# Optimization experiments

Measured on AMD Instinct MI355X. Metric: run time of the kernel, lower is better.

## Reference

```python
import jax, jax.numpy as jnp
import numpy as np

BN_EPS = 1e-5

def _sqdist(a, b):
    # a: (B,N,3), b: (B,M,3) -> (B,N,M)
    return (jnp.sum(a**2, -1)[:, :, None] + jnp.sum(b**2, -1)[:, None, :]
            - 2.0 * jnp.einsum('bnc,bmc->bnm', a, b))

def _knn_idx(pts, k):
    # smallest-k neighbor indices, (B,N,k)
    d = _sqdist(pts, pts)
    _, idx = jax.lax.top_k(-d, k)
    return idx

def _group(feat, idx):
    # feat (B,C,N), idx (B,N,K) -> (B,C,N,K)
    return jax.vmap(lambda f, i: f[:, i])(feat, idx)

def _gather_pts(pts, idx):
    # pts (B,M,C), idx (B,...) -> (B,...,C)
    return jax.vmap(lambda p, i: p[i])(pts, idx)

def _conv1(w, b, x):
    # 1x1 conv1d: w (O,C), x (B,C,N)
    return jnp.einsum('oc,bcn->bon', w, x) + b[None, :, None]

def _conv2(w, x, b=None):
    # 1x1 conv2d: w (O,C), x (B,C,N,K)
    y = jnp.einsum('oc,bcnk->bonk', w, x)
    return y if b is None else y + b[None, :, None, None]

def _bn_eval(x, gamma, beta):
    # eval-mode BatchNorm2d with running_mean=0, running_var=1
    s = gamma / jnp.sqrt(1.0 + BN_EPS)
    return x * s[None, :, None, None] + beta[None, :, None, None]

def _lgrp(x_q, x, P_anchor, map_idx, anchor_dist, lw1, lw2, lw3, k=16):
    # x_q, x: (B,n,3) -> weights (B,dim,n,k)
    d = _sqdist(x_q, x)
    _, idx = jax.lax.top_k(-d, k)                      # (B,n,k)
    neighbors = _gather_pts(x, idx)                    # (B,n,k,3)
    R1 = jnp.abs(x_q[:, :, None, :] - neighbors)       # (B,n,k,3)
    B_idx = _gather_pts(map_idx[..., None], idx)[..., 0]  # (B,n,k)
    anchorA = _gather_pts(P_anchor, map_idx)           # (B,n,3)
    anchorB = _gather_pts(P_anchor, B_idx)             # (B,n,k,3)
    dA = jnp.linalg.norm(x_q - anchorA, axis=-1)       # (B,n)
    dB = jnp.linalg.norm(neighbors - anchorB, axis=-1) # (B,n,k)
    dAB = jax.vmap(lambda ad, a, bi: ad[a[:, None], bi])(anchor_dist, map_idx, B_idx)
    R2s = dA[:, :, None] + dAB + dB                    # (B,n,k)
    R2 = jnp.broadcast_to(R2s[..., None], R1.shape)
    feats = jnp.concatenate([R1, R2], axis=-1).transpose(0, 3, 1, 2)  # (B,6,n,k)
    h = jax.nn.relu(_conv2(lw1, feats))
    h = jax.nn.relu(_conv2(lw2, h))
    return _conv2(lw3, h)                              # (B,dim,n,k)

def setup_inputs() -> dict:
    key = jax.random.key(0)
    ks = jax.random.split(key, 32)
    B, C_in, n, dim, M, k = 2, 128, 2048, 256, 128, 16
    hid_p, hid_a = 64, dim * 4
    s = 0.05
    inp = {
        'x': jax.random.normal(ks[0], (B, C_in, n), jnp.float32),
        'pos': jax.random.normal(ks[1], (B, 3, n), jnp.float32),
        'fps_idx': jax.random.randint(ks[2], (B, n), 0, n),
        'P_anchor': jax.random.normal(ks[3], (B, M, 3), jnp.float32),
        'map_idx': jax.random.randint(ks[4], (B, n), 0, M),
        'anchor_dist': jax.random.uniform(ks[5], (B, M, M), jnp.float32) * 2.0,
        'w_start': jax.random.normal(ks[6], (dim, C_in)) * s,
        'b_start': jnp.zeros((dim,), jnp.float32),
        'w_key': jax.random.normal(ks[7], (dim, dim)) * s,
        'b_key': jnp.zeros((dim,), jnp.float32),
        'w_query': jax.random.normal(ks[8], (dim, dim)) * s,
        'b_query': jnp.zeros((dim,), jnp.float32),
        'w_value': jax.random.normal(ks[9], (dim, dim)) * s,
        'b_value': jnp.zeros((dim,), jnp.float32),
        'pw1': jax.random.normal(ks[10], (hid_p, 3)) * s,
        'pb1': jnp.zeros((hid_p,), jnp.float32),
        'pg1': jnp.ones((hid_p,), jnp.float32),
        'pbt1': jnp.zeros((hid_p,), jnp.float32),
        'pw2': jax.random.normal(ks[11], (dim, hid_p)) * s,
        'pb2': jnp.zeros((dim,), jnp.float32),
        'lw1': jax.random.normal(ks[12], (32, 6)) * s,
        'lw2': jax.random.normal(ks[13], (64, 32)) * s,
        'lw3': jax.random.normal(ks[14], (dim, 64)) * s,
        'aw1': jax.random.normal(ks[15], (hid_a, dim)) * s,
        'ab1': jnp.zeros((hid_a,), jnp.float32),
        'ag1': jnp.ones((hid_a,), jnp.float32),
        'abt1': jnp.zeros((hid_a,), jnp.float32),
        'aw2': jax.random.normal(ks[16], (dim, hid_a)) * s,
        'ab2': jnp.zeros((dim,), jnp.float32),
        'w_end': jax.random.normal(ks[17], (C_in, dim)) * s,
        'b_end': jnp.zeros((C_in,), jnp.float32),
    }
    return inp

def reference(x, pos, fps_idx, P_anchor, map_idx, anchor_dist,
              w_start, b_start, w_key, b_key, w_query, b_query, w_value, b_value,
              pw1, pb1, pg1, pbt1, pw2, pb2, lw1, lw2, lw3,
              aw1, ab1, ag1, abt1, aw2, ab2, w_end, b_end):
    n_knn = 16
    identity = x
    xf = _conv1(w_start, b_start, x)                   # (B,dim,n)
    pos_f = pos.transpose(0, 2, 1)                     # (B,n,3)
    idx_knn = _knn_idx(pos_f, n_knn)                   # (B,n,k)
    key_f = _conv1(w_key, b_key, xf)
    value = _conv1(w_value, b_value, xf)
    query = _conv1(w_query, b_query, xf)
    key_g = _group(key_f, idx_knn)                     # (B,dim,n,k)
    qk_rel = query[:, :, :, None] - key_g
    pos_rel = pos[:, :, :, None] - _group(pos, idx_knn)
    f_l = _lgrp(pos_f, pos_f, P_anchor, map_idx, anchor_dist, lw1, lw2, lw3, k=16)
    # pos_mlp: conv-bn-relu-conv
    h = _bn_eval(_conv2(pw1, pos_rel, pb1), pg1, pbt1)
    pos_emb = _conv2(pw2, jax.nn.relu(h), pb2)         # (B,dim,n,k)
    # attn_mlp
    a = _bn_eval(_conv2(aw1, qk_rel + pos_emb + f_l, ab1), ag1, abt1)
    attention = _conv2(aw2, jax.nn.relu(a), ab2)
    attention = jax.nn.softmax(attention, axis=-1)
    value_e = value[:, :, :, None] + pos_emb + f_l
    agg = jnp.sum(attention * value_e, axis=-1)        # (B,dim,n)
    y = _conv1(w_end, b_end, agg)
    return y + identity
```

## Files before the change

### kernel.cpp

```cpp
#include <hip/hip_runtime.h>
#include <hip/hip_bf16.h>

typedef __hip_bfloat16 bf16;
typedef unsigned short u16;
typedef __attribute__((ext_vector_type(8))) short s8v;
typedef __attribute__((ext_vector_type(4))) float f32x4;

#define NP    2048
#define DC    256
#define MA    128
#define KNN_  16
#define LKV   768

#define MFMA_B16(a,b,c) __builtin_amdgcn_mfma_f32_16x16x32_bf16(a,b,c,0,0,0)

__device__ __forceinline__ float u2f(u16 u){ return __uint_as_float(((unsigned int)u)<<16); }
__device__ __forceinline__ u16 f2u(float f){ bf16 h=__float2bfloat16(f); u16 us; __builtin_memcpy(&us,&h,2); return us; }

__device__ __forceinline__ s8v ldpk(const u16* pk, int rb, int KS, int ks, int l){
  return *(const s8v*)(pk + (((size_t)((rb*KS + ks)*64 + l))<<3));
}

__device__ __forceinline__ s8v ldF(const u16* base, int cf, int ks, int NKS, int l){
  return *(const s8v*)((const char*)base + (((cf*NKS + ks)<<10) | (l<<4)));
}
__device__ __forceinline__ int faddr(int col, int ch, int NKS){
  int cf = col>>4, ks = ch>>5, lane = (((ch>>3)&3)<<4)|(col&15), j = ch&7;
  return ((cf*NKS + ks)<<10) + (lane<<4) + (j<<1);
}
__device__ __forceinline__ void stF4(u16* base, int col, int ch0, int NKS,
                                     float v0, float v1, float v2, float v3){
  uint2 pkv;
  pkv.x = (unsigned)f2u(v0) | ((unsigned)f2u(v1)<<16);
  pkv.y = (unsigned)f2u(v2) | ((unsigned)f2u(v3)<<16);
  *(uint2*)((char*)base + faddr(col, ch0, NKS)) = pkv;
}
__device__ __forceinline__ void stF1(u16* base, int col, int ch, int NKS, float v){
  *(u16*)((char*)base + faddr(col, ch, NKS)) = f2u(v);
}
__device__ __forceinline__ void ldF4(const u16* base, int col, int ch0, int NKS, float* o){
  uint2 pkv = *(const uint2*)((const char*)base + faddr(col, ch0, NKS));
  o[0] = u2f(pkv.x & 0xffff); o[1] = u2f(pkv.x>>16);
  o[2] = u2f(pkv.y & 0xffff); o[3] = u2f(pkv.y>>16);
}

__global__ __launch_bounds__(256) void kqv_fused(
    const u16* __restrict__ wstpk, const float* __restrict__ b_start,
    const u16* __restrict__ wkqvpk, const float* __restrict__ bkqv,
    const float* __restrict__ x, float* __restrict__ kqvT)
{
  __shared__ u16 Bx[64*128];
  __shared__ u16 Bt[64*256];
  const int tid = threadIdx.x;
  const int w = tid>>6, l = tid&63, k = l&15, g = l>>4;
  const int n0 = blockIdx.x*64, m0 = blockIdx.y*128, bb = blockIdx.z;
  for (int e = tid*4; e < 64*128; e += 1024) {
    int kk = e >> 6, c = e & 63;
    float4 v = *(const float4*)(x + (size_t)bb*128*NP + (size_t)kk*NP + n0 + c);
    stF1(Bx, c+0, kk, 4, v.x); stF1(Bx, c+1, kk, 4, v.y);
    stF1(Bx, c+2, kk, 4, v.z); stF1(Bx, c+3, kk, 4, v.w);
  }
  __syncthreads();
  {
    f32x4 accx[4][4];
#pragma unroll
    for (int fr = 0; fr < 4; fr++) {
      int ch0 = w*64 + fr*16 + g*4;
      float4 b4 = *(const float4*)(b_start + ch0);
#pragma unroll
      for (int cf = 0; cf < 4; cf++) {
        accx[fr][cf][0] = b4.x; accx[fr][cf][1] = b4.y;
        accx[fr][cf][2] = b4.z; accx[fr][cf][3] = b4.w;
      }
    }
#pragma unroll
    for (int ks = 0; ks < 4; ks++) {
      s8v aF[4];
#pragma unroll
      for (int fr = 0; fr < 4; fr++) aF[fr] = ldpk(wstpk, w*4 + fr, 4, ks, l);
#pragma unroll
      for (int cf = 0; cf < 4; cf++) {
        s8v bF = ldF(Bx, cf, ks, 4, l);
#pragma unroll
        for (int fr = 0; fr < 4; fr++) accx[fr][cf] = MFMA_B16(aF[fr], bF, accx[fr][cf]);
      }
    }
#pragma unroll
    for (int fr = 0; fr < 4; fr++)
#pragma unroll
      for (int cf = 0; cf < 4; cf++)
        stF4(Bt, cf*16 + k, w*64 + fr*16 + g*4, 8,
             accx[fr][cf][0], accx[fr][cf][1], accx[fr][cf][2], accx[fr][cf][3]);
  }
  __syncthreads();
  f32x4 acc[2][4] = {};
  const int rbase = (m0>>4) + w*2;
#pragma unroll
  for (int ks = 0; ks < 8; ks++) {
    s8v a0 = ldpk(wkqvpk, rbase,   8, ks, l);
    s8v a1 = ldpk(wkqvpk, rbase+1, 8, ks, l);
#pragma unroll
    for (int cf = 0; cf < 4; cf++) {
      s8v bF = ldF(Bt, cf, ks, 8, l);
      acc[0][cf] = MFMA_B16(a0, bF, acc[0][cf]);
      acc[1][cf] = MFMA_B16(a1, bF, acc[1][cf]);
    }
  }
#pragma unroll
  for (int ri = 0; ri < 2; ri++) {
    int mrow = m0 + w*32 + ri*16 + g*4;
    float4 bv = *(const float4*)(bkqv + mrow);
#pragma unroll
    for (int cf = 0; cf < 4; cf++) {
      int n = n0 + cf*16 + k;
      float4 v;
      v.x = acc[ri][cf][0] + bv.x;
      v.y = acc[ri][cf][1] + bv.y;
      v.z = acc[ri][cf][2] + bv.z;
      v.w = acc[ri][cf][3] + bv.w;
      *(float4*)(kqvT + ((size_t)bb*NP + n)*LKV + mrow) = v;
    }
  }
}

__global__ __launch_bounds__(1024) void prep_knn(
    const float* __restrict__ pos, int* __restrict__ idx,
    const float* __restrict__ aw1, const float* __restrict__ aw2,
    const float* __restrict__ lw3, const float* __restrict__ pw2,
    const float* __restrict__ w_start, const float* __restrict__ w_key,
    const float* __restrict__ w_query, const float* __restrict__ w_value,
    const float* __restrict__ w_end,
    const float* __restrict__ b_key, const float* __restrict__ b_query,
    const float* __restrict__ b_value,
    const float* __restrict__ ag1, const float* __restrict__ ab1, const float* __restrict__ abt1,
    const float* __restrict__ pg1, const float* __restrict__ pb1, const float* __restrict__ pbt1,
    u16* __restrict__ aw1pk, u16* __restrict__ aw2pk, u16* __restrict__ wppk,
    u16* __restrict__ wstpk, u16* __restrict__ wkqvpk, u16* __restrict__ wendpk,
    float* __restrict__ sa, float* __restrict__ oa, float* __restrict__ sp,
    float* __restrict__ op_, float* __restrict__ bkqv)
{
  __shared__ float px[NP], py[NP], pz[NP], pn[NP];
  if (blockIdx.x < 256) {
    const int tid = threadIdx.x;
    const int w = tid >> 6, l = tid & 63;
    const int bb = blockIdx.x >> 7;
    const int q0 = (blockIdx.x & 127) * 16;
    const float* pp = pos + (size_t)bb * 3 * NP;
    for (int t = tid; t < NP; t += 1024) {
      float x = pp[t], y = pp[NP + t], z = pp[2*NP + t];
      px[t] = x; py[t] = y; pz[t] = z; pn[t] = x*x + y*y + z*z;
    }
    __syncthreads();
    const int qi = q0 + w;
    const float qx = px[qi], qy = py[qi], qz = pz[qi], qn = pn[qi];
    float bd[16]; int bi[16];
#pragma unroll
    for (int t = 0; t < 16; t++) { bd[t] = 3.4e38f; bi[t] = -1; }
    float worst = 3.4e38f;
    for (int t = 0; t < 32; t++) {
      int j = t*64 + l;
      float d = qn + pn[j] - 2.f * (qx*px[j] + qy*py[j] + qz*pz[j]);
      if (__any(d < worst)) {
        float cd = (d < worst) ? d : 3.4e38f;
        int   cj = j;
#pragma unroll
        for (int s = 0; s < 16; s++) {
          bool sw = cd < bd[s];
          float od = bd[s]; int oj = bi[s];
          bd[s] = sw ? cd : od;  bi[s] = sw ? cj : oj;
          cd    = sw ? od : cd;  cj    = sw ? oj : cj;
        }
        worst = bd[15];
      }
    }
    int myj = 0;
#pragma unroll
    for (int r = 0; r < 16; r++) {
      float md = bd[0]; int mj = bi[0];
#pragma unroll
      for (int o = 1; o < 64; o <<= 1) {
        float od = __shfl_xor(md, o);
        int   oj = __shfl_xor(mj, o);
        bool tk = (od < md) || (od == md && ((unsigned)oj < (unsigned)mj));
        md = tk ? od : md;  mj = tk ? oj : mj;
      }
      if (l == r) myj = mj;
      bool win = (bi[0] == mj);
#pragma unroll
      for (int s = 0; s < 15; s++) {
        bd[s] = win ? bd[s+1] : bd[s];
        bi[s] = win ? bi[s+1] : bi[s];
      }
      bd[15] = win ? 3.4e38f : bd[15];
    }
    if (l < 16) idx[((size_t)bb * NP + qi) * KNN_ + l] = myj;
    return;
  }
  int i = (blockIdx.x - 256) * 1024 + threadIdx.x;
  const float inv = rsqrtf(1.0f + 1e-5f);
  if (i < 262144) {
    int rb = i >> 12, rem = i & 4095, ks = rem >> 9, l = (rem >> 3) & 63, j = rem & 7;
    int row = rb*16 + (l & 15), colk = ks*32 + (l >> 4)*8 + j;
    aw1pk[i] = f2u(aw1[(size_t)row*256 + colk]); return;
  }
  i -= 262144;
  if (i < 262144) {
    int rb = i >> 14, rem = i & 16383, ks = rem >> 9, l = (rem >> 3) & 63, j = rem & 7;
    int row = rb*16 + (l & 15), colk = ks*32 + (l >> 4)*8 + j;
    aw2pk[i] = f2u(aw2[(size_t)row*1024 + colk]); return;
  }
  i -= 262144;
  if (i < 32768) {
    int rb = i >> 11, rem = i & 2047, ks = rem >> 9, l = (rem >> 3) & 63, j = rem & 7;
    int row = rb*16 + (l & 15), colk = ks*32 + (l >> 4)*8 + j;
    float v = (colk < 64) ? lw3[row*64 + colk] : pw2[row*64 + (colk - 64)];
    wppk[i] = f2u(v); return;
  }
  i -= 32768;
  if (i < 32768) {
    int rb = i >> 11, rem = i & 2047, ks = rem >> 9, l = (rem >> 3) & 63, j = rem & 7;
    int row = rb*16 + (l & 15), colk = ks*32 + (l >> 4)*8 + j;
    wstpk[i] = f2u(w_start[(size_t)row*128 + colk]); return;
  }
  i -= 32768;
  if (i < 196608) {
    int rb = i >> 12, rem = i & 4095, ks = rem >> 9, l = (rem >> 3) & 63, j = rem & 7;
    int row = rb*16 + (l & 15), colk = ks*32 + (l >> 4)*8 + j;
    float v = (row < 256) ? w_key[(size_t)row*256 + colk]
            : (row < 512) ? w_query[(size_t)(row-256)*256 + colk]
                          : w_value[(size_t)(row-512)*256 + colk];
    wkqvpk[i] = f2u(v); return;
  }
  i -= 196608;
  if (i < 32768) {
    int rb = i >> 12, rem = i & 4095, ks = rem >> 9, l = (rem >> 3) & 63, j = rem & 7;
    int row = rb*16 + (l & 15), colk = ks*32 + (l >> 4)*8 + j;
    wendpk[i] = f2u(w_end[(size_t)row*256 + colk]); return;
  }
  i -= 32768;
  if (i < 1024) { float s_ = ag1[i]*inv; sa[i] = s_; oa[i] = ab1[i]*s_ + abt1[i]; return; }
  i -= 1024;
  if (i < 64)  { float s_ = pg1[i]*inv; sp[i] = s_; op_[i] = pb1[i]*s_ + pbt1[i]; return; }
  i -= 64;
  if (i < 768) {
    bkqv[i] = (i < 256) ? b_key[i] : (i < 512) ? b_query[i-256] : b_value[i-512];
  }
}

__global__ __launch_bounds__(256, 2) void fused_attn(
    const float* __restrict__ kqv, const int* __restrict__ knn_idx,
    const float* __restrict__ pos, const int* __restrict__ map_idx,
    const float* __restrict__ P_anchor, const float* __restrict__ adist,
    const float* __restrict__ lw1f, const float* __restrict__ lw2f, const float* __restrict__ pw1f,
    const float* __restrict__ spv, const float* __restrict__ opv, const float* __restrict__ pb2f,
    const u16* __restrict__ aw1pk, const float* __restrict__ sav, const float* __restrict__ oav,
    const u16* __restrict__ aw2pk, const u16* __restrict__ wppk, const float* __restrict__ ab2f,
    const u16* __restrict__ wendpk, const float* __restrict__ b_endv,
    const float* __restrict__ xin, float* __restrict__ outp)
{
  __shared__ __align__(16) char smem[65536];
  u16*   s_t   = (u16*)smem;
  u16*   hid0  = (u16*)(smem + 32768);
  u16*   hid1  = (u16*)(smem + 49152);
  float* fFEAT = (float*)smem;
  float* fPREL = (float*)(smem + 1632);
  u16*   fH1   = (u16*) (smem + 2448);

  const int tid = threadIdx.x;
  const int w = tid >> 6, l = tid & 63;
  const int k = l & 15, g = l >> 4;
  const int p0 = blockIdx.x * 4;
  const int b = p0 >> 11, pi0 = p0 & 2047;
  const int pi = pi0 + w;
  const int col_w = w*16 + k;

  const float* kqvB = kqv + (size_t)b * NP * LKV;
  const int* knnB = knn_idx + ((size_t)b * NP) * KNN_;

  if (l < 16) {
    int kk = l;
    int j = knnB[(size_t)pi * KNN_ + kk];
    const float* pp = pos + (size_t)b * 3 * NP;
    float qx = pp[pi], qy = pp[NP+pi], qz = pp[2*NP+pi];
    float nx = pp[j],  ny = pp[NP+j],  nz = pp[2*NP+j];
    float r1x = qx-nx, r1y = qy-ny, r1z = qz-nz;
    fPREL[(w*3+0)*17+kk] = r1x; fPREL[(w*3+1)*17+kk] = r1y; fPREL[(w*3+2)*17+kk] = r1z;
    int mi = map_idx[b*NP + pi];
    int bj = map_idx[b*NP + j];
    const float* pa = P_anchor + (size_t)b * MA * 3;
    float ax = pa[mi*3], ay = pa[mi*3+1], az = pa[mi*3+2];
    float bx = pa[bj*3], by = pa[bj*3+1], bz = pa[bj*3+2];
    float dA = sqrtf((qx-ax)*(qx-ax)+(qy-ay)*(qy-ay)+(qz-az)*(qz-az));
    float dB = sqrtf((nx-bx)*(nx-bx)+(ny-by)*(ny-by)+(nz-bz)*(nz-bz));
    float dAB = adist[(size_t)b*MA*MA + mi*MA + bj];
    float r2 = dA + dAB + dB;
    fFEAT[(w*6+0)*17+kk] = fabsf(r1x); fFEAT[(w*6+1)*17+kk] = fabsf(r1y);
    fFEAT[(w*6+2)*17+kk] = fabsf(r1z);
    fFEAT[(w*6+3)*17+kk] = r2; fFEAT[(w*6+4)*17+kk] = r2; fFEAT[(w*6+5)*17+kk] = r2;
  }
  __syncthreads();

  {
    float f0=fFEAT[(w*6+0)*17+k], f1=fFEAT[(w*6+1)*17+k], f2=fFEAT[(w*6+2)*17+k],
          f3=fFEAT[(w*6+3)*17+k], f4=fFEAT[(w*6+4)*17+k], f5=fFEAT[(w*6+5)*17+k];
#pragma unroll
    for (int jj = 0; jj < 8; jj++) {
      int h = g*8 + jj;
      const float* wp = lw1f + h*6;
      float v = wp[0]*f0 + wp[1]*f1 + wp[2]*f2 + wp[3]*f3 + wp[4]*f4 + wp[5]*f5;
      fH1[(w*32+h)*17+k] = f2u(fmaxf(v, 0.f));
    }
  }
  __syncthreads();

  {
    float hr[32];
#pragma unroll
    for (int t = 0; t < 32; t++) hr[t] = u2f(fH1[(w*32+t)*17+k]);
#pragma unroll
    for (int jj = 0; jj < 16; jj++) {
      int h = g*16 + jj;
      const float4* wp = (const float4*)(lw2f + h*32);
      float a = 0.f;
#pragma unroll
      for (int t4 = 0; t4 < 8; t4++) {
        float4 wv = wp[t4];
        a += wv.x*hr[t4*4] + wv.y*hr[t4*4+1] + wv.z*hr[t4*4+2] + wv.w*hr[t4*4+3];
      }
      stF1(hid0, col_w, h, 4, fmaxf(a, 0.f));
    }
    float pr0 = fPREL[(w*3+0)*17+k], pr1 = fPREL[(w*3+1)*17+k], pr2 = fPREL[(w*3+2)*17+k];
#pragma unroll
    for (int jj = 0; jj < 16; jj++) {
      int h = g*16 + jj;
      float d = pw1f[h*3]*pr0 + pw1f[h*3+1]*pr1 + pw1f[h*3+2]*pr2;
      stF1(hid0, col_w, 64 + h, 4, fmaxf(d*spv[h] + opv[h], 0.f));
    }
  }
  __syncthreads();

  {
    f32x4 accs[4][4];
#pragma unroll
    for (int fr = 0; fr < 4; fr++) {
      int ch0 = w*64 + fr*16 + g*4;
      const float4 p4 = *(const float4*)(pb2f + ch0);
#pragma unroll
      for (int fc = 0; fc < 4; fc++) {
        int j = knnB[(size_t)(pi0 + fc) * KNN_ + k];
        const float4 q4 = *(const float4*)(kqvB + (size_t)(pi0 + fc)*LKV + 256 + ch0);
        const float4 k4 = *(const float4*)(kqvB + (size_t)j*LKV + ch0);
        accs[fr][fc][0] = q4.x - k4.x + p4.x;
        accs[fr][fc][1] = q4.y - k4.y + p4.y;
        accs[fr][fc][2] = q4.z - k4.z + p4.z;
        accs[fr][fc][3] = q4.w - k4.w + p4.w;
      }
    }
#pragma unroll
    for (int ks = 0; ks < 4; ks++) {
      s8v aF[4];
#pragma unroll
      for (int fr = 0; fr < 4; fr++) aF[fr] = ldpk(wppk, w*4 + fr, 4, ks, l);
#pragma unroll
      for (int fc = 0; fc < 4; fc++) {
        s8v bF = ldF(hid0, fc, ks, 4, l);
#pragma unroll
        for (int fr = 0; fr < 4; fr++) accs[fr][fc] = MFMA_B16(aF[fr], bF, accs[fr][fc]);
      }
    }
#pragma unroll
    for (int fr = 0; fr < 4; fr++)
#pragma unroll
      for (int fc = 0; fc < 4; fc++)
        stF4(s_t, fc*16 + k, w*64 + fr*16 + g*4, 8,
             accs[fr][fc][0], accs[fr][fc][1], accs[fr][fc][2], accs[fr][fc][3]);
  }
  __syncthreads();

  f32x4 acc2[4][4];
#pragma unroll
  for (int fr = 0; fr < 4; fr++) {
    const float4 a4 = *(const float4*)(ab2f + w*64 + fr*16 + g*4);
#pragma unroll
    for (int fc = 0; fc < 4; fc++) {
      acc2[fr][fc][0] = a4.x; acc2[fr][fc][1] = a4.y;
      acc2[fr][fc][2] = a4.z; acc2[fr][fc][3] = a4.w;
    }
  }

  {
    f32x4 acc1[2][4] = {};
    const int rb0 = w*2;
    __builtin_amdgcn_s_setprio(1);
#pragma unroll
    for (int ks = 0; ks < 8; ks++) {
      s8v a0 = ldpk(aw1pk, rb0,     8, ks, l);
      s8v a1 = ldpk(aw1pk, rb0 + 1, 8, ks, l);
#pragma unroll
      for (int cf = 0; cf < 4; cf++) {
        s8v bF = ldF(s_t, cf, ks, 8, l);
        acc1[0][cf] = MFMA_B16(a0, bF, acc1[0][cf]);
        acc1[1][cf] = MFMA_B16(a1, bF, acc1[1][cf]);
      }
    }
    __builtin_amdgcn_s_setprio(0);
#pragma unroll
    for (int ri = 0; ri < 2; ri++) {
      int hl = w*32 + ri*16 + g*4;
      const float4 sc = *(const float4*)(sav + hl);
      const float4 of = *(const float4*)(oav + hl);
#pragma unroll
      for (int cf = 0; cf < 4; cf++) {
        float v0 = fmaxf(acc1[ri][cf][0]*sc.x + of.x, 0.f);
        float v1 = fmaxf(acc1[ri][cf][1]*sc.y + of.y, 0.f);
        float v2 = fmaxf(acc1[ri][cf][2]*sc.z + of.z, 0.f);
        float v3 = fmaxf(acc1[ri][cf][3]*sc.w + of.w, 0.f);
        stF4(hid0, cf*16 + k, hl, 4, v0, v1, v2, v3);
      }
    }
  }
  __syncthreads();

  for (int c = 0; c < 8; c++) {
    u16* cur = (c & 1) ? hid1 : hid0;
    u16* nxt = (c & 1) ? hid0 : hid1;
    __builtin_amdgcn_s_setprio(1);
#pragma unroll
    for (int ks = 0; ks < 4; ks++) {
      s8v aF[4];
#pragma unroll
      for (int rf = 0; rf < 4; rf++) aF[rf] = ldpk(aw2pk, w*4 + rf, 32, c*4 + ks, l);
#pragma unroll
      for (int cf = 0; cf < 4; cf++) {
        s8v bF = ldF(cur, cf, ks, 4, l);
#pragma unroll
        for (int rf = 0; rf < 4; rf++) acc2[rf][cf] = MFMA_B16(aF[rf], bF, acc2[rf][cf]);
      }
    }
    __builtin_amdgcn_s_setprio(0);
    if (c < 7) {
      f32x4 acc1[2][4] = {};
      const int rb0 = (c+1)*8 + w*2;
      __builtin_amdgcn_s_setprio(1);
#pragma unroll
      for (int ks = 0; ks < 8; ks++) {
        s8v a0 = ldpk(aw1pk, rb0,     8, ks, l);
        s8v a1 = ldpk(aw1pk, rb0 + 1, 8, ks, l);
#pragma unroll
        for (int cf = 0; cf < 4; cf++) {
          s8v bF = ldF(s_t, cf, ks, 8, l);
          acc1[0][cf] = MFMA_B16(a0, bF, acc1[0][cf]);
          acc1[1][cf] = MFMA_B16(a1, bF, acc1[1][cf]);
        }
      }
      __builtin_amdgcn_s_setprio(0);
#pragma unroll
      for (int ri = 0; ri < 2; ri++) {
        int hl = w*32 + ri*16 + g*4;
        int hg = (c+1)*128 + hl;
        const float4 sc = *(const float4*)(sav + hg);
        const float4 of = *(const float4*)(oav + hg);
#pragma unroll
        for (int cf = 0; cf < 4; cf++) {
          float v0 = fmaxf(acc1[ri][cf][0]*sc.x + of.x, 0.f);
          float v1 = fmaxf(acc1[ri][cf][1]*sc.y + of.y, 0.f);
          float v2 = fmaxf(acc1[ri][cf][2]*sc.z + of.z, 0.f);
          float v3 = fmaxf(acc1[ri][cf][3]*sc.w + of.w, 0.f);
          stF4(nxt, cf*16 + k, hl, 4, v0, v1, v2, v3);
        }
      }
      __syncthreads();
    }
  }

  {
    uint2 z; z.x = 0u; z.y = 0u;
    char* bz = (char*)hid0 + tid*32;
#pragma unroll
    for (int t = 0; t < 4; t++) *(uint2*)(bz + t*8) = z;
  }
  __syncthreads();

#pragma unroll
  for (int fc = 0; fc < 4; fc++) {
    int j = knnB[(size_t)(pi0 + fc) * KNN_ + k];
    const float* qp = kqvB + (size_t)(pi0 + fc)*LKV + 256;
    const float* kp = kqvB + (size_t)j*LKV;
    const float* vp = kqvB + (size_t)(pi0 + fc)*LKV + 512;
#pragma unroll
    for (int fr = 0; fr < 4; fr++) {
      int ch0 = w*64 + fr*16 + g*4;
      float q4[4], k4[4], v4[4], s4[4], res[4];
      *(float4*)q4 = *(const float4*)(qp + ch0);
      *(float4*)k4 = *(const float4*)(kp + ch0);
      *(float4*)v4 = *(const float4*)(vp + ch0);
      ldF4(s_t, fc*16 + k, ch0, 8, s4);
#pragma unroll
      for (int r = 0; r < 4; r++) {
        float a = acc2[fr][fc][r];
        float m = a;
        m = fmaxf(m, __shfl_xor(m, 1, 16)); m = fmaxf(m, __shfl_xor(m, 2, 16));
        m = fmaxf(m, __shfl_xor(m, 4, 16)); m = fmaxf(m, __shfl_xor(m, 8, 16));
        float ex = __expf(a - m);
        float se = ex;
        se += __shfl_xor(se, 1, 16); se += __shfl_xor(se, 2, 16);
        se += __shfl_xor(se, 4, 16); se += __shfl_xor(se, 8, 16);
        float watt = ex / se;
        float ve = v4[r] - q4[r] + s4[r] + k4[r];
        float cc = watt * ve;
        cc += __shfl_xor(cc, 1, 16); cc += __shfl_xor(cc, 2, 16);
        cc += __shfl_xor(cc, 4, 16); cc += __shfl_xor(cc, 8, 16);
        res[r] = cc;
      }
      if (k == 0)
        stF4(hid0, fc, ch0, 8, res[0], res[1], res[2], res[3]);
    }
  }
  __syncthreads();

  {
    f32x4 oacc[2] = {};
#pragma unroll
    for (int ks = 0; ks < 8; ks++) {
      s8v a0 = ldpk(wendpk, w*2 + 0, 8, ks, l);
      s8v a1 = ldpk(wendpk, w*2 + 1, 8, ks, l);
      s8v bF = ldF(hid0, 0, ks, 8, l);
      oacc[0] = MFMA_B16(a0, bF, oacc[0]);
      oacc[1] = MFMA_B16(a1, bF, oacc[1]);
    }
    float* otile = (float*)hid1;
    int p = l & 15, g4 = l >> 4;
    if (p < 4) {
#pragma unroll
      for (int ri = 0; ri < 2; ri++)
#pragma unroll
        for (int r = 0; r < 4; r++) {
          int m = (w*2 + ri)*16 + g4*4 + r;
          otile[m*4 + p] = oacc[ri][r];
        }
    }
    __syncthreads();
    if (tid < 128) {
      int m = tid;
      float4 ov = *(float4*)(otile + m*4);
      size_t o = ((size_t)(b*128) + m)*NP + pi0;
      float4 xv = *(const float4*)(xin + o);
      float be = b_endv[m];
      *(float4*)(outp + o) = make_float4(ov.x+be+xv.x, ov.y+be+xv.y,
                                         ov.z+be+xv.z, ov.w+be+xv.w);
    }
  }
}

extern "C" void kernel_launch(void* const* d_in, const int* in_sizes, int n_in,
                              void* d_out, int out_size, void* d_ws, size_t ws_size,
                              hipStream_t stream)
{
  const float* x        = (const float*)d_in[0];
  const float* pos      = (const float*)d_in[1];
  const float* P_anchor = (const float*)d_in[3];
  const int*   map_idx  = (const int*)  d_in[4];
  const float* adist    = (const float*)d_in[5];
  const float* w_start  = (const float*)d_in[6];
  const float* b_start  = (const float*)d_in[7];
  const float* w_key    = (const float*)d_in[8];
  const float* b_key    = (const float*)d_in[9];
  const float* w_query  = (const float*)d_in[10];
  const float* b_query  = (const float*)d_in[11];
  const float* w_value  = (const float*)d_in[12];
  const float* b_value  = (const float*)d_in[13];
  const float* pw1      = (const float*)d_in[14];
  const float* pb1      = (const float*)d_in[15];
  const float* pg1      = (const float*)d_in[16];
  const float* pbt1     = (const float*)d_in[17];
  const float* pw2      = (const float*)d_in[18];
  const float* pb2      = (const float*)d_in[19];
  const float* lw1      = (const float*)d_in[20];
  const float* lw2      = (const float*)d_in[21];
  const float* lw3      = (const float*)d_in[22];
  const float* aw1      = (const float*)d_in[23];
  const float* ab1      = (const float*)d_in[24];
  const float* ag1      = (const float*)d_in[25];
  const float* abt1     = (const float*)d_in[26];
  const float* aw2      = (const float*)d_in[27];
  const float* ab2      = (const float*)d_in[28];
  const float* w_end    = (const float*)d_in[29];
  const float* b_end    = (const float*)d_in[30];

  if (ws_size < (size_t)4672384 * 4) return;

  float* ws     = (float*)d_ws;
  float* kqvT   = ws + 1048576;
  u16*   aw1pk  = (u16*)(ws + 4194304);
  u16*   aw2pk  = (u16*)(ws + 4325376);
  u16*   wppk   = (u16*)(ws + 4456448);
  u16*   wstpk  = (u16*)(ws + 4472832);
  u16*   wkqvpk = (u16*)(ws + 4489216);
  u16*   wendpk = (u16*)(ws + 4587520);
  float* sa     = ws + 4603904;
  float* oa     = ws + 4604928;
  float* sp     = ws + 4605952;
  float* op_    = ws + 4606016;
  float* bkqv   = ws + 4606080;
  int*   knn_i  = (int*)(ws + 4606848);

  prep_knn<<<1058, 1024, 0, stream>>>(pos, knn_i,
      aw1, aw2, lw3, pw2, w_start, w_key, w_query, w_value, w_end,
      b_key, b_query, b_value, ag1, ab1, abt1, pg1, pb1, pbt1,
      aw1pk, aw2pk, wppk, wstpk, wkqvpk, wendpk, sa, oa, sp, op_, bkqv);

  kqv_fused<<<dim3(32, 6, 2), 256, 0, stream>>>(
      wstpk, b_start, wkqvpk, bkqv, x, kqvT);

  fused_attn<<<1024, 256, 0, stream>>>(kqvT, knn_i,
      pos, map_idx, P_anchor, adist,
      lw1, lw2, pw1, sp, op_, pb2,
      aw1pk, sa, oa, aw2pk, wppk, ab2,
      wendpk, b_end, x, (float*)d_out);
}
```

Baseline: 199.0 us.

## Process eight points per 512-thread block and drop double-buffered hidden pipeline

Each block of the fused attention kernel now handles 8 points with 8 waves instead of 4 points with 4 waves. Every wave covers a narrower channel slice but all 128 neighbor columns, so each packed weight fragment feeds twice as many MFMAs and weight traffic per point drops. The software-pipelined aw1/aw2 chunk loop with ping-pong hidden buffers is replaced by a single hidden buffer and two barriers per chunk. This gives up the overlap between the two GEMMs and raises shared memory use to 96KB per block, which may limit occupancy.

```diff
diff --git a/kernel.cpp b/kernel.cpp
--- a/kernel.cpp
+++ b/kernel.cpp
@@ -247,7 +247,7 @@
   }
 }
 
-__global__ __launch_bounds__(256, 2) void fused_attn(
+__global__ __launch_bounds__(512, 2) void fused_attn(
     const float* __restrict__ kqv, const int* __restrict__ knn_idx,
     const float* __restrict__ pos, const int* __restrict__ map_idx,
     const float* __restrict__ P_anchor, const float* __restrict__ adist,
@@ -258,18 +258,17 @@
     const u16* __restrict__ wendpk, const float* __restrict__ b_endv,
     const float* __restrict__ xin, float* __restrict__ outp)
 {
-  __shared__ __align__(16) char smem[65536];
-  u16*   s_t   = (u16*)smem;
-  u16*   hid0  = (u16*)(smem + 32768);
-  u16*   hid1  = (u16*)(smem + 49152);
+  __shared__ __align__(16) char smem[98304];
+  u16*   s_t  = (u16*)smem;
+  u16*   hid  = (u16*)(smem + 65536);
   float* fFEAT = (float*)smem;
-  float* fPREL = (float*)(smem + 1632);
-  u16*   fH1   = (u16*) (smem + 2448);
+  float* fPREL = (float*)(smem + 3264);
+  u16*   fH1   = (u16*) (smem + 4896);
 
   const int tid = threadIdx.x;
   const int w = tid >> 6, l = tid & 63;
   const int k = l & 15, g = l >> 4;
-  const int p0 = blockIdx.x * 4;
+  const int p0 = blockIdx.x * 8;
   const int b = p0 >> 11, pi0 = p0 & 2047;
   const int pi = pi0 + w;
   const int col_w = w*16 + k;
@@ -327,26 +326,26 @@
         float4 wv = wp[t4];
         a += wv.x*hr[t4*4] + wv.y*hr[t4*4+1] + wv.z*hr[t4*4+2] + wv.w*hr[t4*4+3];
       }
-      stF1(hid0, col_w, h, 4, fmaxf(a, 0.f));
+      stF1(hid, col_w, h, 4, fmaxf(a, 0.f));
     }
     float pr0 = fPREL[(w*3+0)*17+k], pr1 = fPREL[(w*3+1)*17+k], pr2 = fPREL[(w*3+2)*17+k];
 #pragma unroll
     for (int jj = 0; jj < 16; jj++) {
       int h = g*16 + jj;
       float d = pw1f[h*3]*pr0 + pw1f[h*3+1]*pr1 + pw1f[h*3+2]*pr2;
-      stF1(hid0, col_w, 64 + h, 4, fmaxf(d*spv[h] + opv[h], 0.f));
+      stF1(hid, col_w, 64 + h, 4, fmaxf(d*spv[h] + opv[h], 0.f));
     }
   }
   __syncthreads();
 
   {
-    f32x4 accs[4][4];
-#pragma unroll
-    for (int fr = 0; fr < 4; fr++) {
-      int ch0 = w*64 + fr*16 + g*4;
+    f32x4 accs[2][8];
+#pragma unroll
+    for (int fr = 0; fr < 2; fr++) {
+      int ch0 = w*32 + fr*16 + g*4;
       const float4 p4 = *(const float4*)(pb2f + ch0);
 #pragma unroll
-      for (int fc = 0; fc < 4; fc++) {
+      for (int fc = 0; fc < 8; fc++) {
         int j = knnB[(size_t)(pi0 + fc) * KNN_ + k];
         const float4 q4 = *(const float4*)(kqvB + (size_t)(pi0 + fc)*LKV + 256 + ch0);
         const float4 k4 = *(const float4*)(kqvB + (size_t)j*LKV + ch0);
@@ -358,138 +357,93 @@
     }
 #pragma unroll
     for (int ks = 0; ks < 4; ks++) {
-      s8v aF[4];
-#pragma unroll
-      for (int fr = 0; fr < 4; fr++) aF[fr] = ldpk(wppk, w*4 + fr, 4, ks, l);
-#pragma unroll
-      for (int fc = 0; fc < 4; fc++) {
-        s8v bF = ldF(hid0, fc, ks, 4, l);
-#pragma unroll
-        for (int fr = 0; fr < 4; fr++) accs[fr][fc] = MFMA_B16(aF[fr], bF, accs[fr][fc]);
-      }
-    }
-#pragma unroll
-    for (int fr = 0; fr < 4; fr++)
-#pragma unroll
-      for (int fc = 0; fc < 4; fc++)
-        stF4(s_t, fc*16 + k, w*64 + fr*16 + g*4, 8,
+      s8v a0 = ldpk(wppk, w*2 + 0, 4, ks, l);
+      s8v a1 = ldpk(wppk, w*2 + 1, 4, ks, l);
+#pragma unroll
+      for (int fc = 0; fc < 8; fc++) {
+        s8v bF = ldF(hid, fc, ks, 4, l);
+        accs[0][fc] = MFMA_B16(a0, bF, accs[0][fc]);
+        accs[1][fc] = MFMA_B16(a1, bF, accs[1][fc]);
+      }
+    }
+#pragma unroll
+    for (int fr = 0; fr < 2; fr++)
+#pragma unroll
+      for (int fc = 0; fc < 8; fc++)
+        stF4(s_t, fc*16 + k, w*32 + fr*16 + g*4, 8,
              accs[fr][fc][0], accs[fr][fc][1], accs[fr][fc][2], accs[fr][fc][3]);
   }
   __syncthreads();
 
-  f32x4 acc2[4][4];
-#pragma unroll
-  for (int fr = 0; fr < 4; fr++) {
-    const float4 a4 = *(const float4*)(ab2f + w*64 + fr*16 + g*4);
-#pragma unroll
-    for (int fc = 0; fc < 4; fc++) {
+  f32x4 acc2[2][8];
+#pragma unroll
+  for (int fr = 0; fr < 2; fr++) {
+    const float4 a4 = *(const float4*)(ab2f + w*32 + fr*16 + g*4);
+#pragma unroll
+    for (int fc = 0; fc < 8; fc++) {
       acc2[fr][fc][0] = a4.x; acc2[fr][fc][1] = a4.y;
       acc2[fr][fc][2] = a4.z; acc2[fr][fc][3] = a4.w;
     }
   }
 
-  {
-    f32x4 acc1[2][4] = {};
-    const int rb0 = w*2;
+  for (int c = 0; c < 8; c++) {
+    f32x4 acc1[8] = {};
+    const int rb = c*8 + w;
     __builtin_amdgcn_s_setprio(1);
 #pragma unroll
     for (int ks = 0; ks < 8; ks++) {
-      s8v a0 = ldpk(aw1pk, rb0,     8, ks, l);
-      s8v a1 = ldpk(aw1pk, rb0 + 1, 8, ks, l);
-#pragma unroll
-      for (int cf = 0; cf < 4; cf++) {
+      s8v a0 = ldpk(aw1pk, rb, 8, ks, l);
+#pragma unroll
+      for (int cf = 0; cf < 8; cf++) {
         s8v bF = ldF(s_t, cf, ks, 8, l);
-        acc1[0][cf] = MFMA_B16(a0, bF, acc1[0][cf]);
-        acc1[1][cf] = MFMA_B16(a1, bF, acc1[1][cf]);
+        acc1[cf] = MFMA_B16(a0, bF, acc1[cf]);
       }
     }
     __builtin_amdgcn_s_setprio(0);
-#pragma unroll
-    for (int ri = 0; ri < 2; ri++) {
-      int hl = w*32 + ri*16 + g*4;
-      const float4 sc = *(const float4*)(sav + hl);
-      const float4 of = *(const float4*)(oav + hl);
-#pragma unroll
-      for (int cf = 0; cf < 4; cf++) {
-        float v0 = fmaxf(acc1[ri][cf][0]*sc.x + of.x, 0.f);
-        float v1 = fmaxf(acc1[ri][cf][1]*sc.y + of.y, 0.f);
-        float v2 = fmaxf(acc1[ri][cf][2]*sc.z + of.z, 0.f);
-        float v3 = fmaxf(acc1[ri][cf][3]*sc.w + of.w, 0.f);
-        stF4(hid0, cf*16 + k, hl, 4, v0, v1, v2, v3);
-      }
-    }
-  }
-  __syncthreads();
-
-  for (int c = 0; c < 8; c++) {
-    u16* cur = (c & 1) ? hid1 : hid0;
-    u16* nxt = (c & 1) ? hid0 : hid1;
+    __syncthreads();
+    {
+      int hl = w*16 + g*4;
+      int hg = c*128 + hl;
+      const float4 sc = *(const float4*)(sav + hg);
+      const float4 of = *(const float4*)(oav + hg);
+#pragma unroll
+      for (int cf = 0; cf < 8; cf++) {
+        float v0 = fmaxf(acc1[cf][0]*sc.x + of.x, 0.f);
+        float v1 = fmaxf(acc1[cf][1]*sc.y + of.y, 0.f);
+        float v2 = fmaxf(acc1[cf][2]*sc.z + of.z, 0.f);
+        float v3 = fmaxf(acc1[cf][3]*sc.w + of.w, 0.f);
+        stF4(hid, cf*16 + k, hl, 4, v0, v1, v2, v3);
+      }
+    }
+    __syncthreads();
     __builtin_amdgcn_s_setprio(1);
 #pragma unroll
     for (int ks = 0; ks < 4; ks++) {
-      s8v aF[4];
-#pragma unroll
-      for (int rf = 0; rf < 4; rf++) aF[rf] = ldpk(aw2pk, w*4 + rf, 32, c*4 + ks, l);
-#pragma unroll
-      for (int cf = 0; cf < 4; cf++) {
-        s8v bF = ldF(cur, cf, ks, 4, l);
-#pragma unroll
-        for (int rf = 0; rf < 4; rf++) acc2[rf][cf] = MFMA_B16(aF[rf], bF, acc2[rf][cf]);
+      s8v a0 = ldpk(aw2pk, w*2 + 0, 32, c*4 + ks, l);
+      s8v a1 = ldpk(aw2pk, w*2 + 1, 32, c*4 + ks, l);
+#pragma unroll
+      for (int cf = 0; cf < 8; cf++) {
+        s8v bF = ldF(hid, cf, ks, 4, l);
+        acc2[0][cf] = MFMA_B16(a0, bF, acc2[0][cf]);
+        acc2[1][cf] = MFMA_B16(a1, bF, acc2[1][cf]);
       }
     }
     __builtin_amdgcn_s_setprio(0);
-    if (c < 7) {
-      f32x4 acc1[2][4] = {};
-      const int rb0 = (c+1)*8 + w*2;
-      __builtin_amdgcn_s_setprio(1);
-#pragma unroll
-      for (int ks = 0; ks < 8; ks++) {
-        s8v a0 = ldpk(aw1pk, rb0,     8, ks, l);
-        s8v a1 = ldpk(aw1pk, rb0 + 1, 8, ks, l);
-#pragma unroll
-        for (int cf = 0; cf < 4; cf++) {
-          s8v bF = ldF(s_t, cf, ks, 8, l);
-          acc1[0][cf] = MFMA_B16(a0, bF, acc1[0][cf]);
-          acc1[1][cf] = MFMA_B16(a1, bF, acc1[1][cf]);
-        }
-      }
-      __builtin_amdgcn_s_setprio(0);
-#pragma unroll
-      for (int ri = 0; ri < 2; ri++) {
-        int hl = w*32 + ri*16 + g*4;
-        int hg = (c+1)*128 + hl;
-        const float4 sc = *(const float4*)(sav + hg);
-        const float4 of = *(const float4*)(oav + hg);
-#pragma unroll
-        for (int cf = 0; cf < 4; cf++) {
-          float v0 = fmaxf(acc1[ri][cf][0]*sc.x + of.x, 0.f);
-          float v1 = fmaxf(acc1[ri][cf][1]*sc.y + of.y, 0.f);
-          float v2 = fmaxf(acc1[ri][cf][2]*sc.z + of.z, 0.f);
-          float v3 = fmaxf(acc1[ri][cf][3]*sc.w + of.w, 0.f);
-          stF4(nxt, cf*16 + k, hl, 4, v0, v1, v2, v3);
-        }
-      }
-      __syncthreads();
-    }
-  }
-
-  {
-    uint2 z; z.x = 0u; z.y = 0u;
-    char* bz = (char*)hid0 + tid*32;
-#pragma unroll
-    for (int t = 0; t < 4; t++) *(uint2*)(bz + t*8) = z;
-  }
-  __syncthreads();
-
-#pragma unroll
-  for (int fc = 0; fc < 4; fc++) {
+  }
+  __syncthreads();
+
+  *(uint4*)((char*)hid + tid*16) = make_uint4(0,0,0,0);
+  __syncthreads();
+
+#pragma unroll
+  for (int fc = 0; fc < 8; fc++) {
     int j = knnB[(size_t)(pi0 + fc) * KNN_ + k];
     const float* qp = kqvB + (size_t)(pi0 + fc)*LKV + 256;
     const float* kp = kqvB + (size_t)j*LKV;
     const float* vp = kqvB + (size_t)(pi0 + fc)*LKV + 512;
 #pragma unroll
-    for (int fr = 0; fr < 4; fr++) {
-      int ch0 = w*64 + fr*16 + g*4;
+    for (int fr = 0; fr < 2; fr++) {
+      int ch0 = w*32 + fr*16 + g*4;
       float q4[4], k4[4], v4[4], s4[4], res[4];
       *(float4*)q4 = *(const float4*)(qp + ch0);
       *(float4*)k4 = *(const float4*)(kp + ch0);
@@ -513,37 +467,33 @@
         res[r] = cc;
       }
       if (k == 0)
-        stF4(hid0, fc, ch0, 8, res[0], res[1], res[2], res[3]);
+        stF4(hid, fc, ch0, 8, res[0], res[1], res[2], res[3]);
     }
   }
   __syncthreads();
 
   {
-    f32x4 oacc[2] = {};
+    f32x4 oacc = {};
 #pragma unroll
     for (int ks = 0; ks < 8; ks++) {
-      s8v a0 = ldpk(wendpk, w*2 + 0, 8, ks, l);
-      s8v a1 = ldpk(wendpk, w*2 + 1, 8, ks, l);
-      s8v bF = ldF(hid0, 0, ks, 8, l);
-      oacc[0] = MFMA_B16(a0, bF, oacc[0]);
-      oacc[1] = MFMA_B16(a1, bF, oacc[1]);
-    }
-    float* otile = (float*)hid1;
+      s8v a0 = ldpk(wendpk, w, 8, ks, l);
+      s8v bF = ldF(hid, 0, ks, 8, l);
+      oacc = MFMA_B16(a0, bF, oacc);
+    }
+    float* otile = (float*)((char*)hid + 8192);
     int p = l & 15, g4 = l >> 4;
-    if (p < 4) {
-#pragma unroll
-      for (int ri = 0; ri < 2; ri++)
-#pragma unroll
-        for (int r = 0; r < 4; r++) {
-          int m = (w*2 + ri)*16 + g4*4 + r;
-          otile[m*4 + p] = oacc[ri][r];
-        }
+    if (p < 8) {
+#pragma unroll
+      for (int r = 0; r < 4; r++) {
+        int m = w*16 + g4*4 + r;
+        otile[m*8 + p] = oacc[r];
+      }
     }
     __syncthreads();
-    if (tid < 128) {
-      int m = tid;
-      float4 ov = *(float4*)(otile + m*4);
-      size_t o = ((size_t)(b*128) + m)*NP + pi0;
+    if (tid < 256) {
+      int m = tid >> 1, ph = (tid & 1) * 4;
+      size_t o = ((size_t)(b*128) + m)*NP + pi0 + ph;
+      float4 ov = *(float4*)(otile + m*8 + ph);
       float4 xv = *(const float4*)(xin + o);
       float be = b_endv[m];
       *(float4*)(outp + o) = make_float4(ov.x+be+xv.x, ov.y+be+xv.y,
@@ -612,7 +562,7 @@
   kqv_fused<<<dim3(32, 6, 2), 256, 0, stream>>>(
       wstpk, b_start, wkqvpk, bkqv, x, kqvT);
 
-  fused_attn<<<1024, 256, 0, stream>>>(kqvT, knn_i,
+  fused_attn<<<512, 512, 0, stream>>>(kqvT, knn_i,
       pos, map_idx, P_anchor, adist,
       lw1, lw2, pw1, sp, op_, pb2,
       aw1pk, sa, oa, aw2pk, wppk, ab2,
```

After: 202.2 us. About the same (+1.6%).
